# Kernel tuning notes

Hardware: AMD Instinct MI355X
Metric: run time of the kernel (lower is better)

## Reference

```python
import jax, jax.numpy as jnp
import numpy as np

B, C, L, H = 2, 512, 4096, 8
D = C // H  # depth per head


def setup_inputs() -> dict:
    key = jax.random.key(0)
    k1, k2, k3 = jax.random.split(key, 3)
    queries = jax.random.normal(k1, (B, C, L), dtype=jnp.float32)
    mask = jnp.ones((B, L), dtype=jnp.int32)
    # xavier-ish scaling for stability
    Wm = jax.random.normal(k2, (2 * C, C), dtype=jnp.float32) * (1.0 / np.sqrt(C))
    Wq = jax.random.normal(k3, (C, C), dtype=jnp.float32) * (1.0 / np.sqrt(C))
    return {"queries": queries, "mask": mask, "Wm": Wm, "Wq": Wq}


def reference(queries, mask, Wm, Wq):
    # 1x1 conv projections == channel matmuls on [B, C, L]
    q = jnp.einsum('oc,bcl->bol', Wq, queries)   # [B, C, L]
    m = jnp.einsum('oc,bcl->bol', Wm, queries)   # [B, 2C, L]
    # to [B, L, *], split heads -> [B, H, L, D]
    qh = q.transpose(0, 2, 1).reshape(B, L, H, D).transpose(0, 2, 1, 3)
    mem = m.transpose(0, 2, 1)                   # [B, L, 2C]
    k, v = jnp.split(mem, 2, axis=2)             # each [B, L, C]
    kh = k.reshape(B, L, H, D).transpose(0, 2, 1, 3)
    vh = v.reshape(B, L, H, D).transpose(0, 2, 1, 3)
    qh = qh * (D ** -0.5)
    logits = jnp.einsum('bhqd,bhkd->bhqk', qh, kh)          # [B, H, L, L]
    mf = mask.astype(jnp.float32)[:, None, None, :]          # [B, 1, 1, L]
    logits = logits + (-1e30) * (1.0 - mf)
    weights = jax.nn.softmax(logits, axis=-1)                # dropout is identity in eval
    out = jnp.einsum('bhqk,bhkd->bhqd', weights, vh)         # [B, H, L, D]
    # combine heads -> [B, L, C] -> [B, C, L]
    return out.transpose(0, 2, 1, 3).reshape(B, L, C).transpose(0, 2, 1)
```

## Files before the change

kernel.cpp:

```cpp
#include <hip/hip_runtime.h>

#define Bn 2
#define Cn 512
#define Ln 4096
#define Hn 8
#define Dn 64

typedef _Float16 f16;
typedef _Float16 h8 __attribute__((ext_vector_type(8)));
typedef _Float16 h4 __attribute__((ext_vector_type(4)));
typedef _Float16 h2 __attribute__((ext_vector_type(2)));
typedef float f32x4 __attribute__((ext_vector_type(4)));
typedef float f32x16 __attribute__((ext_vector_type(16)));

#define MFMA32(a, b, c) __builtin_amdgcn_mfma_f32_16x16x32_f16(a, b, c, 0, 0, 0)
#define MFMA3216(a, b, c) __builtin_amdgcn_mfma_f32_32x32x16_f16(a, b, c, 0, 0, 0)
#define AS1(p) ((const __attribute__((address_space(1))) void*)(p))
#define AS3(p) ((__attribute__((address_space(3))) void*)(p))

__global__ __launch_bounds__(256) void k_transpose(const float* __restrict__ X,
                                                   f16* __restrict__ Xt) {
  int bid = blockIdx.x;
  int b  = bid >> 9;
  int r  = bid & 511;
  int lt = r >> 3, ct = r & 7;
  int l0 = lt << 6, c0 = ct << 6;
  __shared__ f16 t[64][66];
  int tid = threadIdx.x;
  int lx = tid & 63, cg = tid >> 6;
  const float* xb = X + ((size_t)b * Cn) * Ln;
#pragma unroll
  for (int rr = 0; rr < 16; ++rr) {
    int cl = cg * 16 + rr;
    t[lx][cl] = (f16)xb[(size_t)(c0 + cl) * Ln + l0 + lx];
  }
  __syncthreads();
  f16* xo = Xt + ((size_t)b * Ln + l0) * Cn + c0;
  int cx = tid & 63, lg = tid >> 6;
#pragma unroll
  for (int rr = 0; rr < 16; ++rr) {
    int ll = lg * 16 + rr;
    xo[(size_t)ll * Cn + cx] = t[ll][cx];
  }
}

__global__ __launch_bounds__(256) void k_proj(const float* __restrict__ Wq,
                                              const float* __restrict__ Wm,
                                              const f16* __restrict__ Xt,
                                              f16* __restrict__ Qd,
                                              f16* __restrict__ Kd,
                                              f16* __restrict__ Vv) {
  int bid = blockIdx.x;
  int b = bid / 384;
  int r = bid % 384;
  int mt = r >> 5, nt = r & 31;
  int o0 = mt << 7, l0 = nt << 7;
  __shared__ f16 a_lds[128][40];
  __shared__ f16 b_lds[128][40];
  int tid = threadIdx.x;
  int lane = tid & 63, w = tid >> 6;
  int wr = w >> 1, wc = w & 1;
  f32x4 acc[4][4] = {};

  int sr = tid >> 1;
  int scg = (tid & 1) << 4;
  int o_s = o0 + sr;
  const float* wrow = (o_s < 512) ? (Wq + (size_t)o_s * Cn)
                                  : (Wm + (size_t)(o_s - 512) * Cn);
  const f16* xrow = Xt + ((size_t)b * Ln + l0 + sr) * Cn;

  for (int kt = 0; kt < 16; ++kt) {
    int c0 = kt << 5;
    __syncthreads();
#pragma unroll
    for (int i = 0; i < 4; ++i) {
      float4 w4 = *(const float4*)(wrow + c0 + scg + 4 * i);
      h4 hh = { (f16)w4.x, (f16)w4.y, (f16)w4.z, (f16)w4.w };
      *(h4*)&a_lds[sr][scg + 4 * i] = hh;
    }
#pragma unroll
    for (int i = 0; i < 2; ++i)
      *(h8*)&b_lds[sr][scg + 8 * i] = *(const h8*)(xrow + c0 + scg + 8 * i);
    __syncthreads();

    h8 af[4], bf[4];
#pragma unroll
    for (int mi = 0; mi < 4; ++mi)
      af[mi] = *(const h8*)&a_lds[wr * 64 + mi * 16 + (lane & 15)][(lane >> 4) * 8];
#pragma unroll
    for (int ni = 0; ni < 4; ++ni)
      bf[ni] = *(const h8*)&b_lds[wc * 64 + ni * 16 + (lane & 15)][(lane >> 4) * 8];
#pragma unroll
    for (int mi = 0; mi < 4; ++mi)
#pragma unroll
      for (int ni = 0; ni < 4; ++ni)
        acc[mi][ni] = MFMA32(af[mi], bf[ni], acc[mi][ni]);
  }

  const float QSCALE = 0.18033688011112042f;
  int lrow = (lane >> 4) << 2;
  int lcol = lane & 15;
#pragma unroll
  for (int mi = 0; mi < 4; ++mi) {
    int ob = o0 + wr * 64 + mi * 16 + lrow;
#pragma unroll
    for (int ni = 0; ni < 4; ++ni) {
      int lc = l0 + wc * 64 + ni * 16 + lcol;
      f32x4 a = acc[mi][ni];
      if (ob < 512) {
        int h = ob >> 6, d = ob & 63;
        h4 hh = { (f16)(a[0] * QSCALE), (f16)(a[1] * QSCALE),
                  (f16)(a[2] * QSCALE), (f16)(a[3] * QSCALE) };
        *(h4*)&Qd[(((size_t)b * Hn + h) * Ln + lc) * Dn + d] = hh;
      } else if (ob < 1024) {
        int oc = ob - 512;
        int h = oc >> 6, d = oc & 63;
        h4 hh = { (f16)a[0], (f16)a[1], (f16)a[2], (f16)a[3] };
        *(h4*)&Kd[(((size_t)b * Hn + h) * Ln + lc) * Dn + d] = hh;
      } else {
        int oc = ob - 1024;
#pragma unroll
        for (int rr = 0; rr < 4; ++rr)
          Vv[((size_t)b * Cn + oc + rr) * Ln + lc] = (f16)a[rr];
      }
    }
  }
}

__global__ __launch_bounds__(256, 2) void k_attn(const f16* __restrict__ Qd,
                                                 const f16* __restrict__ Kd,
                                                 const f16* __restrict__ Vv,
                                                 const int* __restrict__ mask,
                                                 float* __restrict__ out) {
  int bid0 = blockIdx.x;
  int bid = (bid0 & 7) * 64 + (bid0 >> 3);
  int bh = bid >> 5, ib = bid & 31;
  int b = bh >> 3, h = bh & 7;
  int tid = threadIdx.x;
  int lane = tid & 63, w = tid >> 6;
  int il = lane & 31, hi = lane >> 5;

  __shared__ __align__(16) f16 kbuf[2][64 * 64];
  __shared__ __align__(16) f16 vbuf[2][64 * 64];

  int qb = ib * 128 + w * 32;
  const f16* qp = Qd + ((size_t)bh * Ln + qb + il) * Dn;
  h8 qreg[4];
#pragma unroll
  for (int dt = 0; dt < 4; ++dt)
    qreg[dt] = *(const h8*)(qp + dt * 16 + hi * 8);

  const int* mbase = mask + (size_t)b * Ln;
  unsigned long long flags;
  {
    const int4* mp = (const int4*)mbase + lane * 16;
    int ac = 1;
#pragma unroll
    for (int q = 0; q < 16; ++q) { int4 v = mp[q]; ac &= v.x & v.y & v.z & v.w; }
    flags = __ballot(ac == 1);
  }

  const f16* kbase = Kd + (size_t)bh * Ln * Dn;
  const f16* vbase = Vv + ((size_t)b * Cn + h * 64) * Ln;
  int koff[2], voff[2];
#pragma unroll
  for (int q = 0; q < 2; ++q) {
    int rr = w * 16 + q * 8 + (lane >> 3);
    int swz = (lane & 7) ^ (rr & 7);
    koff[q] = rr * 64 + swz * 8;
    voff[q] = rr * Ln + swz * 8;
  }

#define STAGE(bufi, t)                                                          \
  {                                                                             \
    _Pragma("unroll")                                                           \
    for (int q = 0; q < 2; ++q) {                                               \
      __builtin_amdgcn_global_load_lds(AS1(kbase + (size_t)(t) * 4096 + koff[q]),\
                                       AS3(&kbuf[bufi][(w * 16 + q * 8) * 64]), \
                                       16, 0, 0);                               \
      __builtin_amdgcn_global_load_lds(AS1(vbase + (size_t)(t) * 64 + voff[q]), \
                                       AS3(&vbuf[bufi][(w * 16 + q * 8) * 64]), \
                                       16, 0, 0);                               \
    }                                                                           \
  }

  f32x16 acc[2] = {};
  float mrow = -1e38f;
  float lsum = 0.f;

  STAGE(0, 0);
  asm volatile("s_waitcnt vmcnt(0)" ::: "memory");
  __builtin_amdgcn_s_barrier();

  int swz7 = il & 7;
  int cur = 0;
  for (int t = 0; t < 64; ++t) {
    if (t < 63) STAGE(cur ^ 1, t + 1);

    const f16* kl = kbuf[cur];
    f32x16 s0 = {}, s1 = {};
    __builtin_amdgcn_s_setprio(1);
#pragma unroll
    for (int dt = 0; dt < 4; ++dt) {
      int c = ((dt * 2 + hi) ^ swz7) << 3;
      h8 ak0 = *(const h8*)&kl[il * 64 + c];
      h8 ak1 = *(const h8*)&kl[(32 + il) * 64 + c];
      s0 = MFMA3216(ak0, qreg[dt], s0);
      s1 = MFMA3216(ak1, qreg[dt], s1);
    }
    __builtin_amdgcn_s_setprio(0);

    if (!((flags >> t) & 1)) {
#pragma unroll
      for (int r = 0; r < 16; ++r) {
        int j = t * 64 + (r & 3) + 8 * (r >> 2) + 4 * hi;
        if (!mbase[j])      s0[r] = -3.0e4f;
        if (!mbase[j + 32]) s1[r] = -3.0e4f;
      }
    }

    float mx;
    {
      float m0 = fmaxf(s0[0], s0[1]), m1 = fmaxf(s0[2], s0[3]);
      float m2 = fmaxf(s0[4], s0[5]), m3 = fmaxf(s0[6], s0[7]);
      float m4 = fmaxf(s0[8], s0[9]), m5 = fmaxf(s0[10], s0[11]);
      float m6 = fmaxf(s0[12], s0[13]), m7 = fmaxf(s0[14], s0[15]);
      float n0 = fmaxf(s1[0], s1[1]), n1 = fmaxf(s1[2], s1[3]);
      float n2 = fmaxf(s1[4], s1[5]), n3 = fmaxf(s1[6], s1[7]);
      float n4 = fmaxf(s1[8], s1[9]), n5 = fmaxf(s1[10], s1[11]);
      float n6 = fmaxf(s1[12], s1[13]), n7 = fmaxf(s1[14], s1[15]);
      float a = fmaxf(fmaxf(m0, m1), fmaxf(m2, m3));
      float b2 = fmaxf(fmaxf(m4, m5), fmaxf(m6, m7));
      float c = fmaxf(fmaxf(n0, n1), fmaxf(n2, n3));
      float d = fmaxf(fmaxf(n4, n5), fmaxf(n6, n7));
      mx = fmaxf(fmaxf(a, b2), fmaxf(c, d));
    }
    mx = fmaxf(mx, __shfl_xor(mx, 32));

    if (__any(mx > mrow + 8.f)) {
      float mn = fmaxf(mrow, mx);
      float al = __builtin_amdgcn_exp2f(mrow - mn);
      lsum *= al;
#pragma unroll
      for (int r = 0; r < 16; ++r) { acc[0][r] *= al; acc[1][r] *= al; }
      mrow = mn;
    }

#pragma unroll
    for (int r = 0; r < 16; ++r) {
      s0[r] = __builtin_amdgcn_exp2f(s0[r] - mrow);
      s1[r] = __builtin_amdgcn_exp2f(s1[r] - mrow);
    }

    float rs = 0.f;
#pragma unroll
    for (int r = 0; r < 16; r += 4) {
      rs += ((s0[r] + s0[r + 1]) + (s0[r + 2] + s0[r + 3]));
      rs += ((s1[r] + s1[r + 1]) + (s1[r + 2] + s1[r + 3]));
    }
    rs += __shfl_xor(rs, 32);
    lsum += rs;

    float dw0[8], dw1[8];
#pragma unroll
    for (int r = 0; r < 16; r += 2) {
      dw0[r >> 1] = __builtin_bit_cast(float, __builtin_amdgcn_cvt_pkrtz(s0[r], s0[r + 1]));
      dw1[r >> 1] = __builtin_bit_cast(float, __builtin_amdgcn_cvt_pkrtz(s1[r], s1[r + 1]));
    }

    h8 pb[4];
#pragma unroll
    for (int jt = 0; jt < 4; ++jt) {
      const float* dd = (jt < 2) ? dw0 : dw1;
      int base = (jt & 1) * 4;
      float x0 = dd[base + 0], x1 = dd[base + 1];
      float y0 = dd[base + 2], y1 = dd[base + 3];
      float v0 = hi ? x0 : y0, v1 = hi ? x1 : y1;
      float p0 = __shfl_xor(v0, 32), p1 = __shfl_xor(v1, 32);
      union { h8 v; float f[4]; } u;
      u.f[0] = hi ? p0 : x0;
      u.f[1] = hi ? p1 : x1;
      u.f[2] = hi ? y0 : p0;
      u.f[3] = hi ? y1 : p1;
      pb[jt] = u.v;
    }

    const f16* vl = vbuf[cur];
    __builtin_amdgcn_s_setprio(1);
#pragma unroll
    for (int dt = 0; dt < 2; ++dt) {
      int rv = dt * 32 + il;
#pragma unroll
      for (int jt = 0; jt < 4; ++jt) {
        h8 av = *(const h8*)&vl[rv * 64 + (((jt * 2 + hi) ^ swz7) << 3)];
        acc[dt] = MFMA3216(av, pb[jt], acc[dt]);
      }
    }
    __builtin_amdgcn_s_setprio(0);

    asm volatile("s_waitcnt vmcnt(0)" ::: "memory");
    __builtin_amdgcn_s_barrier();
    cur ^= 1;
  }

  float inv = 1.f / lsum;
  size_t obase = ((size_t)b * Cn + h * 64) * Ln + qb + il;
#pragma unroll
  for (int dt = 0; dt < 2; ++dt)
#pragma unroll
    for (int r = 0; r < 16; ++r) {
      int d = dt * 32 + (r & 3) + 8 * (r >> 2) + 4 * hi;
      out[obase + (size_t)d * Ln] = acc[dt][r] * inv;
    }
}

extern "C" void kernel_launch(void* const* d_in, const int* in_sizes, int n_in,
                              void* d_out, int out_size, void* d_ws, size_t ws_size,
                              hipStream_t stream) {
  const float* queries = (const float*)d_in[0];
  const int*   mask    = (const int*)d_in[1];
  const float* Wm      = (const float*)d_in[2];
  const float* Wq      = (const float*)d_in[3];
  float* out = (float*)d_out;
  char* ws = (char*)d_ws;
  f16* Xt = (f16*)(ws);
  f16* Qd = (f16*)(ws + 8388608);
  f16* Kd = (f16*)(ws + 16777216);
  f16* Vv = (f16*)(ws + 25165824);

  k_transpose<<<1024, 256, 0, stream>>>(queries, Xt);
  k_proj<<<768, 256, 0, stream>>>(Wq, Wm, Xt, Qd, Kd, Vv);
  k_attn<<<512, 256, 0, stream>>>(Qd, Kd, Vv, mask, out);
}
```

Before: 145.9 us.

## Software-pipeline attention loop with 4-deep LDS ring and QK lookahead

The attention kernel's K/V LDS staging grows from double to quadruple buffering, so loads are issued three tiles ahead and waited on with a partial vmcnt instead of draining all loads every step. The loop is unrolled by two and restructured so the QK^T MFMAs for tile t+1 are issued before the softmax and PV of tile t. This lets matrix work overlap the exp/shuffle-heavy softmax and hides global-load latency. In exchange, LDS per block doubles to 64KB and two live score tiles raise register pressure, which could limit occupancy or cause spills.

```diff
diff --git a/kernel.cpp b/kernel.cpp
--- a/kernel.cpp
+++ b/kernel.cpp
@@ -9,7 +9,6 @@
 typedef _Float16 f16;
 typedef _Float16 h8 __attribute__((ext_vector_type(8)));
 typedef _Float16 h4 __attribute__((ext_vector_type(4)));
-typedef _Float16 h2 __attribute__((ext_vector_type(2)));
 typedef float f32x4 __attribute__((ext_vector_type(4)));
 typedef float f32x16 __attribute__((ext_vector_type(16)));
 
@@ -140,8 +139,8 @@
   int lane = tid & 63, w = tid >> 6;
   int il = lane & 31, hi = lane >> 5;
 
-  __shared__ __align__(16) f16 kbuf[2][64 * 64];
-  __shared__ __align__(16) f16 vbuf[2][64 * 64];
+  __shared__ __align__(16) f16 kbuf[4][64 * 64];
+  __shared__ __align__(16) f16 vbuf[4][64 * 64];
 
   int qb = ib * 128 + w * 32;
   const f16* qp = Qd + ((size_t)bh * Ln + qb + il) * Dn;
@@ -171,147 +170,167 @@
     voff[q] = rr * Ln + swz * 8;
   }
 
-#define STAGE(bufi, t)                                                          \
+#define STAGE(bi, t)                                                            \
   {                                                                             \
     _Pragma("unroll")                                                           \
     for (int q = 0; q < 2; ++q) {                                               \
       __builtin_amdgcn_global_load_lds(AS1(kbase + (size_t)(t) * 4096 + koff[q]),\
-                                       AS3(&kbuf[bufi][(w * 16 + q * 8) * 64]), \
+                                       AS3(&kbuf[bi][(w * 16 + q * 8) * 64]),   \
                                        16, 0, 0);                               \
       __builtin_amdgcn_global_load_lds(AS1(vbase + (size_t)(t) * 64 + voff[q]), \
-                                       AS3(&vbuf[bufi][(w * 16 + q * 8) * 64]), \
+                                       AS3(&vbuf[bi][(w * 16 + q * 8) * 64]),   \
                                        16, 0, 0);                               \
     }                                                                           \
   }
 
-  f32x16 acc[2] = {};
+  f32x16 acc0 = {}, acc1 = {};
   float mrow = -1e38f;
   float lsum = 0.f;
+  int swz7 = il & 7;
+
+#define QK_TILE(KL, SN0, SN1)                                    \
+  {                                                              \
+    const f16* kl_ = (KL);                                       \
+    f32x16 z0 = {}, z1 = {};                                     \
+    _Pragma("unroll")                                            \
+    for (int dt = 0; dt < 4; ++dt) {                             \
+      int c = ((dt * 2 + hi) ^ swz7) << 3;                       \
+      h8 ak0 = *(const h8*)&kl_[il * 64 + c];                    \
+      h8 ak1 = *(const h8*)&kl_[(32 + il) * 64 + c];             \
+      z0 = MFMA3216(ak0, qreg[dt], z0);                          \
+      z1 = MFMA3216(ak1, qreg[dt], z1);                          \
+    }                                                            \
+    SN0 = z0; SN1 = z1;                                          \
+  }
+
+#define MASK_FIX(tt, S0, S1)                                     \
+  if (!((flags >> (tt)) & 1)) {                                  \
+    _Pragma("unroll")                                            \
+    for (int r = 0; r < 16; ++r) {                               \
+      int j = (tt) * 64 + (r & 3) + 8 * (r >> 2) + 4 * hi;       \
+      if (!mbase[j])      S0[r] = -3.0e4f;                       \
+      if (!mbase[j + 32]) S1[r] = -3.0e4f;                       \
+    }                                                            \
+  }
+
+#define SOFTMAX_PV(tt, S0, S1)                                                  \
+  {                                                                             \
+    float m0 = fmaxf(fmaxf(S0[0], S0[1]), fmaxf(S0[2], S0[3]));                 \
+    float m1 = fmaxf(fmaxf(S0[4], S0[5]), fmaxf(S0[6], S0[7]));                 \
+    float m2 = fmaxf(fmaxf(S0[8], S0[9]), fmaxf(S0[10], S0[11]));               \
+    float m3 = fmaxf(fmaxf(S0[12], S0[13]), fmaxf(S0[14], S0[15]));             \
+    float m4 = fmaxf(fmaxf(S1[0], S1[1]), fmaxf(S1[2], S1[3]));                 \
+    float m5 = fmaxf(fmaxf(S1[4], S1[5]), fmaxf(S1[6], S1[7]));                 \
+    float m6 = fmaxf(fmaxf(S1[8], S1[9]), fmaxf(S1[10], S1[11]));               \
+    float m7 = fmaxf(fmaxf(S1[12], S1[13]), fmaxf(S1[14], S1[15]));             \
+    float mx = fmaxf(fmaxf(fmaxf(m0, m1), fmaxf(m2, m3)),                       \
+                     fmaxf(fmaxf(m4, m5), fmaxf(m6, m7)));                      \
+    mx = fmaxf(mx, __shfl_xor(mx, 32));                                         \
+    if (__any(mx > mrow + 8.f)) {                     \
+      float mn = fmaxf(mrow, mx);                                               \
+      float al = __builtin_amdgcn_exp2f(mrow - mn);                             \
+      lsum *= al;                                                               \
+      _Pragma("unroll")                                                         \
+      for (int r = 0; r < 16; ++r) { acc0[r] *= al; acc1[r] *= al; }            \
+      mrow = mn;                                                                \
+    }                                                                           \
+    _Pragma("unroll")                                                           \
+    for (int r = 0; r < 16; ++r) {                                              \
+      S0[r] = __builtin_amdgcn_exp2f(S0[r] - mrow);                             \
+      S1[r] = __builtin_amdgcn_exp2f(S1[r] - mrow);                             \
+    }                                                                           \
+    {                                           \
+      float a0 = (S0[0] + S0[1]) + (S0[2] + S0[3]);                             \
+      float a1 = (S0[4] + S0[5]) + (S0[6] + S0[7]);                             \
+      float a2 = (S0[8] + S0[9]) + (S0[10] + S0[11]);                           \
+      float a3 = (S0[12] + S0[13]) + (S0[14] + S0[15]);                         \
+      float a4 = (S1[0] + S1[1]) + (S1[2] + S1[3]);                             \
+      float a5 = (S1[4] + S1[5]) + (S1[6] + S1[7]);                             \
+      float a6 = (S1[8] + S1[9]) + (S1[10] + S1[11]);                           \
+      float a7 = (S1[12] + S1[13]) + (S1[14] + S1[15]);                         \
+      float rs = ((a0 + a1) + (a2 + a3)) + ((a4 + a5) + (a6 + a7));             \
+      rs += __shfl_xor(rs, 32);                                                 \
+      lsum += rs;                                                               \
+    }                                                                           \
+    float dw0[8], dw1[8];                                                       \
+    _Pragma("unroll")                                                           \
+    for (int r = 0; r < 16; r += 2) {                                           \
+      dw0[r >> 1] = __builtin_bit_cast(float,                                   \
+          __builtin_amdgcn_cvt_pkrtz(S0[r], S0[r + 1]));                        \
+      dw1[r >> 1] = __builtin_bit_cast(float,                                   \
+          __builtin_amdgcn_cvt_pkrtz(S1[r], S1[r + 1]));                        \
+    }                                                                           \
+    h8 pb[4];                                                                   \
+    _Pragma("unroll")                                                           \
+    for (int jt = 0; jt < 4; ++jt) {                                            \
+      const float* dd = (jt < 2) ? dw0 : dw1;                                   \
+      int base = (jt & 1) * 4;                                                  \
+      float x0 = dd[base + 0], x1 = dd[base + 1];                               \
+      float y0 = dd[base + 2], y1 = dd[base + 3];                               \
+      float v0 = hi ? x0 : y0, v1 = hi ? x1 : y1;                               \
+      float p0 = __shfl_xor(v0, 32), p1 = __shfl_xor(v1, 32);                   \
+      union { h8 v; float f[4]; } u;                                            \
+      u.f[0] = hi ? p0 : x0;                                                    \
+      u.f[1] = hi ? p1 : x1;                                                    \
+      u.f[2] = hi ? y0 : p0;                                                    \
+      u.f[3] = hi ? y1 : p1;                                                    \
+      pb[jt] = u.v;                                                             \
+    }                                                                           \
+    const f16* vl_ = &vbuf[(tt) & 3][0];                                        \
+    __builtin_amdgcn_s_setprio(1);                                              \
+    _Pragma("unroll")                                                           \
+    for (int dt = 0; dt < 2; ++dt) {                                            \
+      int rv = dt * 32 + il;                                                    \
+      _Pragma("unroll")                                                         \
+      for (int jt = 0; jt < 4; ++jt) {                                          \
+        h8 av = *(const h8*)&vl_[rv * 64 + (((jt * 2 + hi) ^ swz7) << 3)];      \
+        if (dt == 0) acc0 = MFMA3216(av, pb[jt], acc0);                         \
+        else         acc1 = MFMA3216(av, pb[jt], acc1);                         \
+      }                                                                         \
+    }                                                                           \
+    __builtin_amdgcn_s_setprio(0);                                              \
+  }
+
+#define BODY(tt, SC0, SC1, SN0, SN1)                                            \
+  {                                                                             \
+    asm volatile("s_waitcnt vmcnt(4)" ::: "memory");                            \
+    __builtin_amdgcn_s_barrier();                                               \
+    if ((tt) + 3 < 64) STAGE(((tt) + 3) & 3, (tt) + 3);                         \
+    QK_TILE(&kbuf[((tt) + 1) & 3][0], SN0, SN1);                                \
+    MASK_FIX((tt) + 1, SN0, SN1);                                               \
+    SOFTMAX_PV(tt, SC0, SC1);                                                   \
+  }
 
   STAGE(0, 0);
-  asm volatile("s_waitcnt vmcnt(0)" ::: "memory");
+  STAGE(1, 1);
+  STAGE(2, 2);
+  asm volatile("s_waitcnt vmcnt(8)" ::: "memory");
   __builtin_amdgcn_s_barrier();
-
-  int swz7 = il & 7;
-  int cur = 0;
-  for (int t = 0; t < 64; ++t) {
-    if (t < 63) STAGE(cur ^ 1, t + 1);
-
-    const f16* kl = kbuf[cur];
-    f32x16 s0 = {}, s1 = {};
-    __builtin_amdgcn_s_setprio(1);
-#pragma unroll
-    for (int dt = 0; dt < 4; ++dt) {
-      int c = ((dt * 2 + hi) ^ swz7) << 3;
-      h8 ak0 = *(const h8*)&kl[il * 64 + c];
-      h8 ak1 = *(const h8*)&kl[(32 + il) * 64 + c];
-      s0 = MFMA3216(ak0, qreg[dt], s0);
-      s1 = MFMA3216(ak1, qreg[dt], s1);
-    }
-    __builtin_amdgcn_s_setprio(0);
-
-    if (!((flags >> t) & 1)) {
-#pragma unroll
-      for (int r = 0; r < 16; ++r) {
-        int j = t * 64 + (r & 3) + 8 * (r >> 2) + 4 * hi;
-        if (!mbase[j])      s0[r] = -3.0e4f;
-        if (!mbase[j + 32]) s1[r] = -3.0e4f;
-      }
-    }
-
-    float mx;
-    {
-      float m0 = fmaxf(s0[0], s0[1]), m1 = fmaxf(s0[2], s0[3]);
-      float m2 = fmaxf(s0[4], s0[5]), m3 = fmaxf(s0[6], s0[7]);
-      float m4 = fmaxf(s0[8], s0[9]), m5 = fmaxf(s0[10], s0[11]);
-      float m6 = fmaxf(s0[12], s0[13]), m7 = fmaxf(s0[14], s0[15]);
-      float n0 = fmaxf(s1[0], s1[1]), n1 = fmaxf(s1[2], s1[3]);
-      float n2 = fmaxf(s1[4], s1[5]), n3 = fmaxf(s1[6], s1[7]);
-      float n4 = fmaxf(s1[8], s1[9]), n5 = fmaxf(s1[10], s1[11]);
-      float n6 = fmaxf(s1[12], s1[13]), n7 = fmaxf(s1[14], s1[15]);
-      float a = fmaxf(fmaxf(m0, m1), fmaxf(m2, m3));
-      float b2 = fmaxf(fmaxf(m4, m5), fmaxf(m6, m7));
-      float c = fmaxf(fmaxf(n0, n1), fmaxf(n2, n3));
-      float d = fmaxf(fmaxf(n4, n5), fmaxf(n6, n7));
-      mx = fmaxf(fmaxf(a, b2), fmaxf(c, d));
-    }
-    mx = fmaxf(mx, __shfl_xor(mx, 32));
-
-    if (__any(mx > mrow + 8.f)) {
-      float mn = fmaxf(mrow, mx);
-      float al = __builtin_amdgcn_exp2f(mrow - mn);
-      lsum *= al;
-#pragma unroll
-      for (int r = 0; r < 16; ++r) { acc[0][r] *= al; acc[1][r] *= al; }
-      mrow = mn;
-    }
-
-#pragma unroll
-    for (int r = 0; r < 16; ++r) {
-      s0[r] = __builtin_amdgcn_exp2f(s0[r] - mrow);
-      s1[r] = __builtin_amdgcn_exp2f(s1[r] - mrow);
-    }
-
-    float rs = 0.f;
-#pragma unroll
-    for (int r = 0; r < 16; r += 4) {
-      rs += ((s0[r] + s0[r + 1]) + (s0[r + 2] + s0[r + 3]));
-      rs += ((s1[r] + s1[r + 1]) + (s1[r + 2] + s1[r + 3]));
-    }
-    rs += __shfl_xor(rs, 32);
-    lsum += rs;
-
-    float dw0[8], dw1[8];
-#pragma unroll
-    for (int r = 0; r < 16; r += 2) {
-      dw0[r >> 1] = __builtin_bit_cast(float, __builtin_amdgcn_cvt_pkrtz(s0[r], s0[r + 1]));
-      dw1[r >> 1] = __builtin_bit_cast(float, __builtin_amdgcn_cvt_pkrtz(s1[r], s1[r + 1]));
-    }
-
-    h8 pb[4];
-#pragma unroll
-    for (int jt = 0; jt < 4; ++jt) {
-      const float* dd = (jt < 2) ? dw0 : dw1;
-      int base = (jt & 1) * 4;
-      float x0 = dd[base + 0], x1 = dd[base + 1];
-      float y0 = dd[base + 2], y1 = dd[base + 3];
-      float v0 = hi ? x0 : y0, v1 = hi ? x1 : y1;
-      float p0 = __shfl_xor(v0, 32), p1 = __shfl_xor(v1, 32);
-      union { h8 v; float f[4]; } u;
-      u.f[0] = hi ? p0 : x0;
-      u.f[1] = hi ? p1 : x1;
-      u.f[2] = hi ? y0 : p0;
-      u.f[3] = hi ? y1 : p1;
-      pb[jt] = u.v;
-    }
-
-    const f16* vl = vbuf[cur];
-    __builtin_amdgcn_s_setprio(1);
-#pragma unroll
-    for (int dt = 0; dt < 2; ++dt) {
-      int rv = dt * 32 + il;
-#pragma unroll
-      for (int jt = 0; jt < 4; ++jt) {
-        h8 av = *(const h8*)&vl[rv * 64 + (((jt * 2 + hi) ^ swz7) << 3)];
-        acc[dt] = MFMA3216(av, pb[jt], acc[dt]);
-      }
-    }
-    __builtin_amdgcn_s_setprio(0);
-
+  f32x16 sE0, sE1, sO0, sO1;
+  QK_TILE(&kbuf[0][0], sE0, sE1);
+  MASK_FIX(0, sE0, sE1);
+
+  for (int t = 0; t < 62; t += 2) {
+    BODY(t, sE0, sE1, sO0, sO1);
+    BODY(t + 1, sO0, sO1, sE0, sE1);
+  }
+  {
     asm volatile("s_waitcnt vmcnt(0)" ::: "memory");
     __builtin_amdgcn_s_barrier();
-    cur ^= 1;
-  }
+    QK_TILE(&kbuf[3][0], sO0, sO1);
+    MASK_FIX(63, sO0, sO1);
+    SOFTMAX_PV(62, sE0, sE1);
+  }
+  SOFTMAX_PV(63, sO0, sO1);
 
   float inv = 1.f / lsum;
   size_t obase = ((size_t)b * Cn + h * 64) * Ln + qb + il;
 #pragma unroll
-  for (int dt = 0; dt < 2; ++dt)
-#pragma unroll
-    for (int r = 0; r < 16; ++r) {
-      int d = dt * 32 + (r & 3) + 8 * (r >> 2) + 4 * hi;
-      out[obase + (size_t)d * Ln] = acc[dt][r] * inv;
-    }
+  for (int r = 0; r < 16; ++r) {
+    int d0 = (r & 3) + 8 * (r >> 2) + 4 * hi;
+    out[obase + (size_t)d0 * Ln] = acc0[r] * inv;
+    out[obase + (size_t)(d0 + 32) * Ln] = acc1[r] * inv;
+  }
 }
 
 extern "C" void kernel_launch(void* const* d_in, const int* in_sizes, int n_in,
```

New measurement: 145.6 us. About the same (-0.2%).
